# Kernel tuning notes

Hardware: AMD Instinct MI355X
Metric: run time of the kernel (lower is better)

The kernel has to match this reference:

```python
import jax, jax.numpy as jnp
import numpy as np

N_A, N_P, E, H, L = 50000, 100000, 500000, 256, 3


def setup_inputs() -> dict:
    key = jax.random.key(0)
    ks = jax.random.split(key, 8)

    def edges(k, n_src, n_dst):
        k1, k2 = jax.random.split(k)
        src = jax.random.randint(k1, (E,), 0, n_src, dtype=jnp.int64 if jax.config.jax_enable_x64 else jnp.int32)
        dst = jax.random.randint(k2, (E,), 0, n_dst, dtype=src.dtype)
        return jnp.stack([src, dst])  # [2, E]

    scale = 1.0 / np.sqrt(H).astype(np.float32)
    return {
        "x_author": jax.random.normal(ks[0], (N_A, H), jnp.float32),
        "x_paper": jax.random.normal(ks[1], (N_P, H), jnp.float32),
        "edge_writes": edges(ks[2], N_A, N_P),   # author -> paper
        "edge_rev": edges(ks[3], N_P, N_A),      # paper  -> author
        "edge_cites": edges(ks[4], N_P, N_P),    # paper  -> paper
        # per-layer, per-edge-type SAGEConv params: [L, n_edge_types=3, ...]
        "Wl": jax.random.normal(ks[5], (L, 3, H, H), jnp.float32) * scale,  # neighbor lin (with bias)
        "bl": jnp.zeros((L, 3, H), jnp.float32),
        "Wr": jax.random.normal(ks[6], (L, 3, H, H), jnp.float32) * scale,  # root lin (no bias)
    }


def _sage(x_src, x_dst, edge, Wl, bl, Wr):
    # SAGEConv: lin_l(mean_{j->i} x_src[j]) + lin_r(x_dst)
    src, dst = edge[0], edge[1]
    n_dst = x_dst.shape[0]
    msum = jax.ops.segment_sum(x_src[src], dst, num_segments=n_dst)        # [n_dst, H]
    cnt = jax.ops.segment_sum(jnp.ones(src.shape, x_src.dtype), dst, num_segments=n_dst)
    mean = msum / jnp.maximum(cnt, 1.0)[:, None]  # nodes with no in-edges stay 0
    return mean @ Wl + bl + x_dst @ Wr


def reference(x_author, x_paper, edge_writes, edge_rev, edge_cites, Wl, bl, Wr):
    xa, xp = x_author, x_paper
    for l in range(L):  # fixed small layer loop
        # HeteroConv aggr='sum' over edge types sharing dst node type
        out_p = _sage(xa, xp, edge_writes, Wl[l, 0], bl[l, 0], Wr[l, 0]) \
              + _sage(xp, xp, edge_cites, Wl[l, 2], bl[l, 2], Wr[l, 2])
        out_a = _sage(xp, xa, edge_rev, Wl[l, 1], bl[l, 1], Wr[l, 1])
        xa, xp = out_a, out_p
    return xa, xp
```

## Files before the change

kernel.cpp:

```cpp
#include <hip/hip_runtime.h>
#include <hip/hip_bf16.h>
#include <cstdint>
#include <cstddef>

#define NA 50000
#define NP 100000
#define HH 256
#define LL 3
#define GP8 12500
#define GA8 6250

typedef __attribute__((ext_vector_type(8))) short short8;
typedef __attribute__((ext_vector_type(4))) float f32x4;

__device__ __forceinline__ float bf2f(unsigned int u16) {
    unsigned int x = u16 << 16;
    return __builtin_bit_cast(float, x);
}
__device__ __forceinline__ unsigned short f2bf(float f) {
    __hip_bfloat16 h = __float2bfloat16(f);
    return __builtin_bit_cast(unsigned short, h);
}

__global__ void prep_w_k(const float* __restrict__ Wl, const float* __restrict__ Wr,
                         unsigned short* __restrict__ WT) {
    int gid = blockIdx.x * 256 + threadIdx.x;
    int w = gid >> 16;
    int within = gid & 65535;
    int n = within >> 8, k = within & 255;
    int l = w / 5, t = w % 5;
    float v;
    if (t == 0)      v = Wl[(size_t)((l * 3 + 0) * 256 + k) * 256 + n];
    else if (t == 1) v = Wl[(size_t)((l * 3 + 2) * 256 + k) * 256 + n];
    else if (t == 2) v = Wr[(size_t)((l * 3 + 0) * 256 + k) * 256 + n] +
                         Wr[(size_t)((l * 3 + 2) * 256 + k) * 256 + n];
    else if (t == 3) v = Wl[(size_t)((l * 3 + 1) * 256 + k) * 256 + n];
    else             v = Wr[(size_t)((l * 3 + 1) * 256 + k) * 256 + n];
    WT[(size_t)w * 65536 + n * 256 + k] = f2bf(v);
}

__global__ void prep_bias_k(const float* __restrict__ bl,
                            float* __restrict__ biasP, float* __restrict__ biasA) {
    int gid = blockIdx.x * 256 + threadIdx.x;
    int l = gid >> 8, n = gid & 255;
    biasP[l * 256 + n] = bl[(l * 3 + 0) * 256 + n] + bl[(l * 3 + 2) * 256 + n];
    biasA[l * 256 + n] = bl[(l * 3 + 1) * 256 + n];
}

__global__ void count3_k(const int* __restrict__ dw, const int* __restrict__ dc,
                         const int* __restrict__ dr, int* __restrict__ cnt,
                         int E, int egrid) {
    int b = blockIdx.x;
    int type = b / egrid, lb = b - type * egrid;
    int e = lb * 256 + threadIdx.x;
    if (e >= E) return;
    const int* d = (type == 0) ? dw : (type == 1) ? dc : dr;
    int base = (type == 0) ? 0 : (type == 1) ? NP : 2 * NP;
    atomicAdd(&cnt[base + d[e]], 1);
}

__global__ void scanA_k(const int* __restrict__ cnt, int* __restrict__ part,
                        int nbP, int nbA) {
    int b = blockIdx.x;
    int type, lb;
    if (b < nbP) { type = 0; lb = b; }
    else if (b < 2 * nbP) { type = 1; lb = b - nbP; }
    else { type = 2; lb = b - 2 * nbP; }
    int n = (type < 2) ? NP : NA;
    int base = (type == 0) ? 0 : (type == 1) ? NP : 2 * NP;
    __shared__ int sh[256];
    int i = lb * 256 + threadIdx.x;
    sh[threadIdx.x] = (i < n) ? cnt[base + i] : 0;
    __syncthreads();
    for (int s = 128; s > 0; s >>= 1) {
        if (threadIdx.x < s) sh[threadIdx.x] += sh[threadIdx.x + s];
        __syncthreads();
    }
    if (threadIdx.x == 0) part[type * 512 + lb] = sh[0];
}
__global__ void scanB_k(int* __restrict__ part, int nbP, int nbA) {
    int type = blockIdx.x;
    int nb = (type < 2) ? nbP : nbA;
    int* seg = part + type * 512;
    __shared__ int sh[512];
    int t = threadIdx.x;
    int v0 = (t < nb) ? seg[t] : 0;
    sh[t] = v0;
    __syncthreads();
    for (int off = 1; off < 512; off <<= 1) {
        int x = (t >= off) ? sh[t - off] : 0;
        __syncthreads();
        sh[t] += x;
        __syncthreads();
    }
    if (t < nb) seg[t] = sh[t] - v0;
}
__global__ void scanC_k(const int* __restrict__ cnt, const int* __restrict__ part,
                        int* __restrict__ rp_w, int* __restrict__ rp_c,
                        int* __restrict__ rp_r, int nbP, int nbA) {
    int b = blockIdx.x;
    int type, lb;
    if (b < nbP) { type = 0; lb = b; }
    else if (b < 2 * nbP) { type = 1; lb = b - nbP; }
    else { type = 2; lb = b - 2 * nbP; }
    int n = (type < 2) ? NP : NA;
    int base = (type == 0) ? 0 : (type == 1) ? NP : 2 * NP;
    int* rowptr = (type == 0) ? rp_w : (type == 1) ? rp_c : rp_r;
    __shared__ int sh[256];
    int t = threadIdx.x;
    int i = lb * 256 + t;
    int v = (i < n) ? cnt[base + i] : 0;
    sh[t] = v;
    __syncthreads();
    for (int off = 1; off < 256; off <<= 1) {
        int x = (t >= off) ? sh[t - off] : 0;
        __syncthreads();
        if (t >= off) sh[t] += x;
        __syncthreads();
    }
    if (i < n) {
        int incl = sh[t];
        int pb = part[type * 512 + lb];
        rowptr[i] = pb + incl - v;
        if (i == n - 1) rowptr[n] = pb + incl;
    }
}
__global__ void fill3_k(const int* __restrict__ e_w, const int* __restrict__ e_c,
                        const int* __restrict__ e_r,
                        const int* __restrict__ rp_w, const int* __restrict__ rp_c,
                        const int* __restrict__ rp_r,
                        int* __restrict__ cursor,
                        int* __restrict__ col_w, int* __restrict__ col_c,
                        int* __restrict__ col_r, int E, int egrid) {
    int b = blockIdx.x;
    int type = b / egrid, lb = b - type * egrid;
    int e = lb * 256 + threadIdx.x;
    if (e >= E) return;
    const int* ep = (type == 0) ? e_w : (type == 1) ? e_c : e_r;
    const int* rowptr = (type == 0) ? rp_w : (type == 1) ? rp_c : rp_r;
    int* col = (type == 0) ? col_w : (type == 1) ? col_c : col_r;
    int base = (type == 0) ? 0 : (type == 1) ? NP : 2 * NP;
    int s = ep[e], d = ep[E + e];
    int pos = atomicAdd(&cursor[base + d], 1);
    col[rowptr[d] + pos] = s;
}

__global__ void cast_bf16_k(const float* __restrict__ x, unsigned short* __restrict__ o, int n8) {
    int g = blockIdx.x * 256 + threadIdx.x;
    if (g >= n8) return;
    const float4* xp = reinterpret_cast<const float4*>(x) + (size_t)g * 2;
    float4 a = xp[0], b = xp[1];
    union { unsigned short u[8]; uint4 v; } r;
    r.u[0] = f2bf(a.x); r.u[1] = f2bf(a.y); r.u[2] = f2bf(a.z); r.u[3] = f2bf(a.w);
    r.u[4] = f2bf(b.x); r.u[5] = f2bf(b.y); r.u[6] = f2bf(b.z); r.u[7] = f2bf(b.w);
    reinterpret_cast<uint4*>(o)[g] = r.v;
}

__global__ void agg_fused_k(const unsigned short* __restrict__ xa,
                            const unsigned short* __restrict__ xp,
                            const int* __restrict__ rp_w, const int* __restrict__ col_w,
                            const int* __restrict__ rp_c, const int* __restrict__ col_c,
                            const int* __restrict__ rp_r, const int* __restrict__ col_r,
                            unsigned short* __restrict__ mW,
                            unsigned short* __restrict__ mC,
                            unsigned short* __restrict__ mR) {
    int b = blockIdx.x;
    const unsigned short* x; const int* rp; const int* cl; unsigned short* mn; int nd;
    if (b < GP8)            { x = xa; rp = rp_w; cl = col_w; mn = mW; nd = NP; }
    else if (b < 2 * GP8)   { b -= GP8; x = xp; rp = rp_c; cl = col_c; mn = mC; nd = NP; }
    else                    { b -= 2 * GP8; x = xp; rp = rp_r; cl = col_r; mn = mR; nd = NA; }
    int node = b * 8 + (threadIdx.x >> 5);
    if (node >= nd) return;
    const int l32 = threadIdx.x & 31;
    int beg = rp[node], end = rp[node + 1];
    int deg = end - beg;
    float a0 = 0.f, a1 = 0.f, a2 = 0.f, a3 = 0.f, a4 = 0.f, a5 = 0.f, a6 = 0.f, a7 = 0.f;
    for (int base = 0; base < deg; base += 32) {
        int n = min(deg - base, 32);
        int myc = (base + l32 < deg) ? cl[beg + base + l32] : 0;
        int i = 0;
        for (; i + 1 < n; i += 2) {
            int s0 = __shfl(myc, i, 32);
            int s1 = __shfl(myc, i + 1, 32);
            uint4 v0 = *reinterpret_cast<const uint4*>(x + (size_t)s0 * 256 + l32 * 8);
            uint4 v1 = *reinterpret_cast<const uint4*>(x + (size_t)s1 * 256 + l32 * 8);
            a0 += bf2f(v0.x & 0xffffu); a1 += bf2f(v0.x >> 16);
            a2 += bf2f(v0.y & 0xffffu); a3 += bf2f(v0.y >> 16);
            a4 += bf2f(v0.z & 0xffffu); a5 += bf2f(v0.z >> 16);
            a6 += bf2f(v0.w & 0xffffu); a7 += bf2f(v0.w >> 16);
            a0 += bf2f(v1.x & 0xffffu); a1 += bf2f(v1.x >> 16);
            a2 += bf2f(v1.y & 0xffffu); a3 += bf2f(v1.y >> 16);
            a4 += bf2f(v1.z & 0xffffu); a5 += bf2f(v1.z >> 16);
            a6 += bf2f(v1.w & 0xffffu); a7 += bf2f(v1.w >> 16);
        }
        if (i < n) {
            int s0 = __shfl(myc, i, 32);
            uint4 v0 = *reinterpret_cast<const uint4*>(x + (size_t)s0 * 256 + l32 * 8);
            a0 += bf2f(v0.x & 0xffffu); a1 += bf2f(v0.x >> 16);
            a2 += bf2f(v0.y & 0xffffu); a3 += bf2f(v0.y >> 16);
            a4 += bf2f(v0.z & 0xffffu); a5 += bf2f(v0.z >> 16);
            a6 += bf2f(v0.w & 0xffffu); a7 += bf2f(v0.w >> 16);
        }
    }
    float sc = (deg > 0) ? 1.0f / (float)deg : 0.f;
    uint4 r;
    r.x = (unsigned int)f2bf(a0 * sc) | ((unsigned int)f2bf(a1 * sc) << 16);
    r.y = (unsigned int)f2bf(a2 * sc) | ((unsigned int)f2bf(a3 * sc) << 16);
    r.z = (unsigned int)f2bf(a4 * sc) | ((unsigned int)f2bf(a5 * sc) << 16);
    r.w = (unsigned int)f2bf(a6 * sc) | ((unsigned int)f2bf(a7 * sc) << 16);
    *reinterpret_cast<uint4*>(mn + (size_t)node * 256 + l32 * 8) = r;
}

#define EP_STRIDE 128
template <bool LAST>
__global__ __launch_bounds__(512, 2)
void gemm_fat_k(const unsigned short* __restrict__ mW, const unsigned short* __restrict__ mC,
                const unsigned short* __restrict__ xp, const unsigned short* __restrict__ mR,
                const unsigned short* __restrict__ xa, const unsigned short* __restrict__ WT_l,
                const float* __restrict__ biasP, const float* __restrict__ biasA,
                void* __restrict__ outP, void* __restrict__ outA, int mtP) {
    __shared__ char lds[128 * EP_STRIDE * 4];
    char* bsh = lds;
    float* eps = reinterpret_cast<float*>(lds);
    const int tid = threadIdx.x;

    const bool isP = (int)blockIdx.x < mtP;
    const int tile = isP ? blockIdx.x : blockIdx.x - mtP;
    const int parts = isP ? 3 : 2;
    const unsigned short* A0 = isP ? mW : mR;
    const unsigned short* A1 = isP ? mC : xa;
    const unsigned short* A2 = xp;
    const unsigned short* WTj = isP ? WT_l : WT_l + 3 * 65536;
    const float* bias = isP ? biasP : biasA;
    void* out = isP ? outP : outA;
    const int M = isP ? NP : NA;

    const int wid = tid >> 6;
    const int l = tid & 63;
    const int kgrp = (l >> 4) << 3;
    int row = tile * 128 + (wid << 4) + (l & 15);
    int rowc = row < M ? row : M - 1;

    f32x4 acc[2][8];
    #pragma unroll
    for (int h = 0; h < 2; ++h)
        #pragma unroll
        for (int t = 0; t < 8; ++t) acc[h][t] = f32x4{0.f, 0.f, 0.f, 0.f};

    bool first = true;
    for (int p = 0; p < parts; ++p) {
        const unsigned short* Ap = (p == 0) ? A0 : (p == 1) ? A1 : A2;
        uint4 a4[8];
        const unsigned short* Arow = Ap + (size_t)rowc * 256 + kgrp;
        #pragma unroll
        for (int s = 0; s < 8; ++s)
            a4[s] = *reinterpret_cast<const uint4*>(Arow + s * 32);

        #pragma unroll
        for (int h = 0; h < 2; ++h) {
            if (!first) __syncthreads();
            first = false;
            const unsigned short* Wt = WTj + (size_t)p * 65536 + h * (128 * 256);
            #pragma unroll
            for (int i = 0; i < 8; ++i) {
                int byte = (i * 512 + tid) * 16;
                uint4 v = *reinterpret_cast<const uint4*>((const char*)Wt + byte);
                *reinterpret_cast<uint4*>(bsh + (byte ^ (((byte >> 9) & 7) << 4))) = v;
            }
            __syncthreads();
            #pragma unroll
            for (int s = 0; s < 8; ++s) {
                short8 a = __builtin_bit_cast(short8, a4[s]);
                #pragma unroll
                for (int t = 0; t < 8; ++t) {
                    int nl = (t << 4) + (l & 15);
                    int byte = (nl * 512 + s * 64 + kgrp * 2) ^ ((nl & 7) << 4);
                    short8 bfr = __builtin_bit_cast(short8, *reinterpret_cast<const uint4*>(bsh + byte));
                    acc[h][t] = __builtin_amdgcn_mfma_f32_16x16x32_bf16(a, bfr, acc[h][t], 0, 0, 0);
                }
            }
        }
    }

    const int col = l & 15;
    const int rloc0 = (wid << 4) + ((l >> 4) << 2);
    #pragma unroll
    for (int h = 0; h < 2; ++h) {
        __syncthreads();
        #pragma unroll
        for (int t = 0; t < 8; ++t) {
            int gc = (h << 7) + (t << 4) + col;
            float badd = bias[gc];
            #pragma unroll
            for (int j = 0; j < 4; ++j)
                eps[(rloc0 + j) * EP_STRIDE + (t << 4) + col] = acc[h][t][j] + badd;
        }
        __syncthreads();
        if (LAST) {
            float* fout = reinterpret_cast<float*>(out);
            #pragma unroll
            for (int i = 0; i < 8; ++i) {
                int c = i * 512 + tid;
                int r = c >> 5, within = c & 31;
                int rg = tile * 128 + r;
                if (rg < M) {
                    const float* src = eps + r * EP_STRIDE + within * 4;
                    float4 v = *reinterpret_cast<const float4*>(src);
                    *reinterpret_cast<float4*>(fout + (size_t)rg * 256 + (h << 7) + within * 4) = v;
                }
            }
        } else {
            unsigned short* bout = reinterpret_cast<unsigned short*>(out);
            #pragma unroll
            for (int i = 0; i < 4; ++i) {
                int c = i * 512 + tid;
                int r = c >> 4, within = c & 15;
                int rg = tile * 128 + r;
                if (rg < M) {
                    const float* src = eps + r * EP_STRIDE + within * 8;
                    float4 lo = *reinterpret_cast<const float4*>(src);
                    float4 hi = *reinterpret_cast<const float4*>(src + 4);
                    uint4 v;
                    v.x = (unsigned int)f2bf(lo.x) | ((unsigned int)f2bf(lo.y) << 16);
                    v.y = (unsigned int)f2bf(lo.z) | ((unsigned int)f2bf(lo.w) << 16);
                    v.z = (unsigned int)f2bf(hi.x) | ((unsigned int)f2bf(hi.y) << 16);
                    v.w = (unsigned int)f2bf(hi.z) | ((unsigned int)f2bf(hi.w) << 16);
                    *reinterpret_cast<uint4*>(bout + (size_t)rg * 256 + (h << 7) + within * 8) = v;
                }
            }
        }
    }
}

extern "C" void kernel_launch(void* const* d_in, const int* in_sizes, int n_in,
                              void* d_out, int out_size, void* d_ws, size_t ws_size,
                              hipStream_t stream) {
    const float* x_author = (const float*)d_in[0];
    const float* x_paper  = (const float*)d_in[1];
    const int* e_w = (const int*)d_in[2];
    const int* e_r = (const int*)d_in[3];
    const int* e_c = (const int*)d_in[4];
    const float* Wl = (const float*)d_in[5];
    const float* bl = (const float*)d_in[6];
    const float* Wr = (const float*)d_in[7];
    const int E = in_sizes[2] / 2;

    float* outA = (float*)d_out;
    float* outP = (float*)d_out + (size_t)NA * HH;

    size_t off = 0;
    auto carve = [&](size_t bytes) {
        void* p = (char*)d_ws + off;
        off += (bytes + 255) & ~(size_t)255;
        return p;
    };
    unsigned short* xa0   = (unsigned short*)carve((size_t)NA * HH * 2);
    unsigned short* xp0   = (unsigned short*)carve((size_t)NP * HH * 2);
    unsigned short* meanW = (unsigned short*)carve((size_t)NP * HH * 2);
    unsigned short* meanC = (unsigned short*)carve((size_t)NP * HH * 2);
    unsigned short* meanR = (unsigned short*)carve((size_t)NA * HH * 2);
    unsigned short* WT    = (unsigned short*)carve((size_t)15 * 65536 * 2);
    float* biasP = (float*)carve((size_t)LL * HH * 4);
    float* biasA = (float*)carve((size_t)LL * HH * 4);
    int* cnt    = (int*)carve((size_t)(2 * NP + NA) * 4);
    int* rp_w   = (int*)carve((size_t)(NP + 1) * 4);
    int* rp_c   = (int*)carve((size_t)(NP + 1) * 4);
    int* rp_r   = (int*)carve((size_t)(NA + 1) * 4);
    int* part   = (int*)carve((size_t)2048 * 4);
    int* col_w  = (int*)carve((size_t)E * 4);
    int* col_c  = (int*)carve((size_t)E * 4);
    int* col_r  = (int*)carve((size_t)E * 4);
    (void)off; (void)ws_size; (void)n_in; (void)out_size;

    const size_t cntBytes = (size_t)(2 * NP + NA) * 4;
    const int egrid = (E + 255) / 256;
    const int nbP = (NP + 255) / 256, nbA = (NA + 255) / 256;
    const int mtP = (NP + 127) / 128, mtA = (NA + 127) / 128;

    hipMemsetAsync(cnt, 0, cntBytes, stream);
    prep_w_k<<<3840, 256, 0, stream>>>(Wl, Wr, WT);
    prep_bias_k<<<3, 256, 0, stream>>>(bl, biasP, biasA);
    count3_k<<<3 * egrid, 256, 0, stream>>>(e_w + E, e_c + E, e_r + E, cnt, E, egrid);
    scanA_k<<<2 * nbP + nbA, 256, 0, stream>>>(cnt, part, nbP, nbA);
    scanB_k<<<3, 512, 0, stream>>>(part, nbP, nbA);
    scanC_k<<<2 * nbP + nbA, 256, 0, stream>>>(cnt, part, rp_w, rp_c, rp_r, nbP, nbA);
    hipMemsetAsync(cnt, 0, cntBytes, stream);
    fill3_k<<<3 * egrid, 256, 0, stream>>>(e_w, e_c, e_r, rp_w, rp_c, rp_r,
                                           cnt, col_w, col_c, col_r, E, egrid);

    cast_bf16_k<<<(NA * HH / 8 + 255) / 256, 256, 0, stream>>>(x_author, xa0, NA * HH / 8);
    cast_bf16_k<<<(NP * HH / 8 + 255) / 256, 256, 0, stream>>>(x_paper, xp0, NP * HH / 8);

    unsigned short* xa1 = (unsigned short*)d_out;
    unsigned short* xp1 = xa1 + (size_t)NA * HH;

    unsigned short* xa_cur = xa0; unsigned short* xp_cur = xp0;
    unsigned short* xa_nxt = xa1; unsigned short* xp_nxt = xp1;

    const int aggGrid = 2 * GP8 + GA8;

    for (int l = 0; l < LL; ++l) {
        const unsigned short* WT_l = WT + (size_t)l * 5 * 65536;
        agg_fused_k<<<aggGrid, 256, 0, stream>>>(xa_cur, xp_cur, rp_w, col_w,
                                                 rp_c, col_c, rp_r, col_r,
                                                 meanW, meanC, meanR);
        if (l < LL - 1) {
            gemm_fat_k<false><<<mtP + mtA, 512, 0, stream>>>(
                meanW, meanC, xp_cur, meanR, xa_cur, WT_l,
                biasP + l * 256, biasA + l * 256, xp_nxt, xa_nxt, mtP);
            unsigned short* t;
            t = xa_cur; xa_cur = xa_nxt; xa_nxt = t;
            t = xp_cur; xp_cur = xp_nxt; xp_nxt = t;
        } else {
            gemm_fat_k<true><<<mtP + mtA, 512, 0, stream>>>(
                meanW, meanC, xp_cur, meanR, xa_cur, WT_l,
                biasP + l * 256, biasA + l * 256, outP, outA, mtP);
        }
    }
}
```

Baseline: 910.2 us.

## Double-buffer K-sliced weight tiles in LDS and use 2x2 warp tiling in GEMM

```diff
diff --git a/kernel.cpp b/kernel.cpp
--- a/kernel.cpp
+++ b/kernel.cpp
@@ -36,7 +36,7 @@
                          Wr[(size_t)((l * 3 + 2) * 256 + k) * 256 + n];
     else if (t == 3) v = Wl[(size_t)((l * 3 + 1) * 256 + k) * 256 + n];
     else             v = Wr[(size_t)((l * 3 + 1) * 256 + k) * 256 + n];
-    WT[(size_t)w * 65536 + n * 256 + k] = f2bf(v);
+    WT[(size_t)w * 65536 + (size_t)(k >> 6) * 16384 + n * 64 + (k & 63)] = f2bf(v);
 }
 
 __global__ void prep_bias_k(const float* __restrict__ bl,
@@ -211,7 +211,6 @@
     *reinterpret_cast<uint4*>(mn + (size_t)node * 256 + l32 * 8) = r;
 }
 
-#define EP_STRIDE 128
 template <bool LAST>
 __global__ __launch_bounds__(512, 2)
 void gemm_fat_k(const unsigned short* __restrict__ mW, const unsigned short* __restrict__ mC,
@@ -219,8 +218,7 @@
                 const unsigned short* __restrict__ xa, const unsigned short* __restrict__ WT_l,
                 const float* __restrict__ biasP, const float* __restrict__ biasA,
                 void* __restrict__ outP, void* __restrict__ outA, int mtP) {
-    __shared__ char lds[128 * EP_STRIDE * 4];
-    char* bsh = lds;
+    __shared__ char lds[65536];
     float* eps = reinterpret_cast<float*>(lds);
     const int tid = threadIdx.x;
 
@@ -230,70 +228,120 @@
     const unsigned short* A0 = isP ? mW : mR;
     const unsigned short* A1 = isP ? mC : xa;
     const unsigned short* A2 = xp;
-    const unsigned short* WTj = isP ? WT_l : WT_l + 3 * 65536;
+    const char* Wb = reinterpret_cast<const char*>(isP ? WT_l : WT_l + 3 * 65536);
     const float* bias = isP ? biasP : biasA;
     void* out = isP ? outP : outA;
     const int M = isP ? NP : NA;
-
-    const int wid = tid >> 6;
-    const int l = tid & 63;
+    const int G = parts * 4;
+
+    const int wid = tid >> 6, l = tid & 63;
+    const int rw = wid & 3, cw = wid >> 2;
     const int kgrp = (l >> 4) << 3;
-    int row = tile * 128 + (wid << 4) + (l & 15);
-    int rowc = row < M ? row : M - 1;
+
+    int row0 = tile * 128 + rw * 32 + (l & 15);
+    int rc0 = row0 < M ? row0 : M - 1;
+    int r1 = row0 + 16;
+    int rc1 = r1 < M ? r1 : M - 1;
+
+    int lwb[4];
+    #pragma unroll
+    for (int i = 0; i < 4; ++i) {
+        int lb = (i * 512 + tid) * 16;
+        lwb[i] = lb ^ (((lb >> 7) & 7) << 4);
+    }
 
     f32x4 acc[2][8];
     #pragma unroll
-    for (int h = 0; h < 2; ++h)
+    for (int f = 0; f < 2; ++f)
         #pragma unroll
-        for (int t = 0; t < 8; ++t) acc[h][t] = f32x4{0.f, 0.f, 0.f, 0.f};
-
-    bool first = true;
+        for (int t = 0; t < 8; ++t) acc[f][t] = f32x4{0.f, 0.f, 0.f, 0.f};
+
+    uint4 sr[4];
+    uint4 afr[2][2][2];
+
+    #pragma unroll
+    for (int i = 0; i < 4; ++i)
+        sr[i] = *reinterpret_cast<const uint4*>(Wb + (i * 512 + tid) * 16);
+    #pragma unroll
+    for (int i = 0; i < 4; ++i)
+        *reinterpret_cast<uint4*>(lds + lwb[i]) = sr[i];
+    #pragma unroll
+    for (int i = 0; i < 4; ++i)
+        sr[i] = *reinterpret_cast<const uint4*>(Wb + 32768 + (i * 512 + tid) * 16);
+    {
+        const unsigned short* b0 = A0 + (size_t)rc0 * 256 + kgrp;
+        const unsigned short* b1 = A0 + (size_t)rc1 * 256 + kgrp;
+        afr[0][0][0] = *reinterpret_cast<const uint4*>(b0);
+        afr[0][0][1] = *reinterpret_cast<const uint4*>(b0 + 32);
+        afr[0][1][0] = *reinterpret_cast<const uint4*>(b1);
+        afr[0][1][1] = *reinterpret_cast<const uint4*>(b1 + 32);
+    }
+    __syncthreads();
+
     for (int p = 0; p < parts; ++p) {
-        const unsigned short* Ap = (p == 0) ? A0 : (p == 1) ? A1 : A2;
-        uint4 a4[8];
-        const unsigned short* Arow = Ap + (size_t)rowc * 256 + kgrp;
         #pragma unroll
-        for (int s = 0; s < 8; ++s)
-            a4[s] = *reinterpret_cast<const uint4*>(Arow + s * 32);
-
-        #pragma unroll
-        for (int h = 0; h < 2; ++h) {
-            if (!first) __syncthreads();
-            first = false;
-            const unsigned short* Wt = WTj + (size_t)p * 65536 + h * (128 * 256);
+        for (int h4 = 0; h4 < 4; ++h4) {
+            const int g = p * 4 + h4;
+            const int cur = h4 & 1;
+            if (g + 1 < G) {
+                const int kq1 = (h4 + 1) & 3;
+                const unsigned short* Apn;
+                if (h4 == 3) Apn = (p + 1 == 1) ? A1 : A2;
+                else         Apn = (p == 0) ? A0 : (p == 1) ? A1 : A2;
+                const unsigned short* b0 = Apn + (size_t)rc0 * 256 + kq1 * 64 + kgrp;
+                const unsigned short* b1 = Apn + (size_t)rc1 * 256 + kq1 * 64 + kgrp;
+                afr[cur ^ 1][0][0] = *reinterpret_cast<const uint4*>(b0);
+                afr[cur ^ 1][0][1] = *reinterpret_cast<const uint4*>(b0 + 32);
+                afr[cur ^ 1][1][0] = *reinterpret_cast<const uint4*>(b1);
+                afr[cur ^ 1][1][1] = *reinterpret_cast<const uint4*>(b1 + 32);
+            }
+            const char* rbuf = lds + cur * 32768;
             #pragma unroll
-            for (int i = 0; i < 8; ++i) {
-                int byte = (i * 512 + tid) * 16;
-                uint4 v = *reinterpret_cast<const uint4*>((const char*)Wt + byte);
-                *reinterpret_cast<uint4*>(bsh + (byte ^ (((byte >> 9) & 7) << 4))) = v;
-            }
-            __syncthreads();
-            #pragma unroll
-            for (int s = 0; s < 8; ++s) {
-                short8 a = __builtin_bit_cast(short8, a4[s]);
+            for (int ks = 0; ks < 2; ++ks) {
+                short8 a0 = __builtin_bit_cast(short8, afr[cur][0][ks]);
+                short8 a1 = __builtin_bit_cast(short8, afr[cur][1][ks]);
                 #pragma unroll
                 for (int t = 0; t < 8; ++t) {
-                    int nl = (t << 4) + (l & 15);
-                    int byte = (nl * 512 + s * 64 + kgrp * 2) ^ ((nl & 7) << 4);
-                    short8 bfr = __builtin_bit_cast(short8, *reinterpret_cast<const uint4*>(bsh + byte));
-                    acc[h][t] = __builtin_amdgcn_mfma_f32_16x16x32_bf16(a, bfr, acc[h][t], 0, 0, 0);
+                    int n = cw * 128 + t * 16 + (l & 15);
+                    int byte = (n * 128 + ks * 64 + kgrp * 2) ^ ((n & 7) << 4);
+                    short8 b = __builtin_bit_cast(short8, *reinterpret_cast<const uint4*>(rbuf + byte));
+                    acc[0][t] = __builtin_amdgcn_mfma_f32_16x16x32_bf16(a0, b, acc[0][t], 0, 0, 0);
+                    acc[1][t] = __builtin_amdgcn_mfma_f32_16x16x32_bf16(a1, b, acc[1][t], 0, 0, 0);
                 }
             }
-        }
-    }
-
-    const int col = l & 15;
-    const int rloc0 = (wid << 4) + ((l >> 4) << 2);
-    #pragma unroll
-    for (int h = 0; h < 2; ++h) {
-        __syncthreads();
-        #pragma unroll
-        for (int t = 0; t < 8; ++t) {
-            int gc = (h << 7) + (t << 4) + col;
-            float badd = bias[gc];
+            if (g + 1 < G) {
+                char* wbuf = lds + (cur ^ 1) * 32768;
+                #pragma unroll
+                for (int i = 0; i < 4; ++i)
+                    *reinterpret_cast<uint4*>(wbuf + lwb[i]) = sr[i];
+            }
+            __syncthreads();
+            if (g + 2 < G) {
+                #pragma unroll
+                for (int i = 0; i < 4; ++i)
+                    sr[i] = *reinterpret_cast<const uint4*>(Wb + (size_t)(g + 2) * 32768 + (i * 512 + tid) * 16);
+            }
+        }
+    }
+
+    const int col16 = l & 15;
+    const int rq = (l >> 4) << 2;
+    #pragma unroll
+    for (int e = 0; e < 2; ++e) {
+        __syncthreads();
+        if (cw == e) {
             #pragma unroll
-            for (int j = 0; j < 4; ++j)
-                eps[(rloc0 + j) * EP_STRIDE + (t << 4) + col] = acc[h][t][j] + badd;
+            for (int f = 0; f < 2; ++f) {
+                #pragma unroll
+                for (int t = 0; t < 8; ++t) {
+                    int lr0 = rw * 32 + f * 16 + rq;
+                    int lc = t * 16 + col16;
+                    float badd = bias[(e << 7) + lc];
+                    #pragma unroll
+                    for (int j = 0; j < 4; ++j)
+                        eps[(lr0 + j) * 128 + lc] = acc[f][t][j] + badd;
+                }
+            }
         }
         __syncthreads();
         if (LAST) {
@@ -304,9 +352,8 @@
                 int r = c >> 5, within = c & 31;
                 int rg = tile * 128 + r;
                 if (rg < M) {
-                    const float* src = eps + r * EP_STRIDE + within * 4;
-                    float4 v = *reinterpret_cast<const float4*>(src);
-                    *reinterpret_cast<float4*>(fout + (size_t)rg * 256 + (h << 7) + within * 4) = v;
+                    float4 v = *reinterpret_cast<const float4*>(eps + r * 128 + within * 4);
+                    *reinterpret_cast<float4*>(fout + (size_t)rg * 256 + (e << 7) + within * 4) = v;
                 }
             }
         } else {
@@ -317,7 +364,7 @@
                 int r = c >> 4, within = c & 15;
                 int rg = tile * 128 + r;
                 if (rg < M) {
-                    const float* src = eps + r * EP_STRIDE + within * 8;
+                    const float* src = eps + r * 128 + within * 8;
                     float4 lo = *reinterpret_cast<const float4*>(src);
                     float4 hi = *reinterpret_cast<const float4*>(src + 4);
                     uint4 v;
@@ -325,7 +372,7 @@
                     v.y = (unsigned int)f2bf(lo.z) | ((unsigned int)f2bf(lo.w) << 16);
                     v.z = (unsigned int)f2bf(hi.x) | ((unsigned int)f2bf(hi.y) << 16);
                     v.w = (unsigned int)f2bf(hi.z) | ((unsigned int)f2bf(hi.w) << 16);
-                    *reinterpret_cast<uint4*>(bout + (size_t)rg * 256 + (h << 7) + within * 8) = v;
+                    *reinterpret_cast<uint4*>(bout + (size_t)rg * 256 + (e << 7) + within * 8) = v;
                 }
             }
         }
```

After: 1.041 ms. 1.14x slower.
